# Kernel optimization log

Measured on AMD Instinct MI355X. Metric: run time of the kernel, lower is better.

The kernel has to match this reference:

```python
import jax, jax.numpy as jnp
import numpy as np

B, S, D, H = 2, 2048, 2048, 16
HD = D // H  # 128 head dim


def setup_inputs() -> dict:
    key = jax.random.key(0)
    k1, k2, k3 = jax.random.split(key, 3)
    x = jax.random.normal(k1, (B, S, D), dtype=jnp.float32)
    w_qkv = jax.random.normal(k2, (3 * D, D), dtype=jnp.float32) * 0.02
    w_out = jax.random.normal(k3, (D, D), dtype=jnp.float32) * 0.02
    # complex-like RoPE table: freqs_cis[s, j] = exp(i * s * theta^{-2j/hd})
    theta = 10000.0
    inv_freq = 1.0 / (theta ** (jnp.arange(0, HD, 2, dtype=jnp.float32) / HD))  # [HD/2]
    t = jnp.arange(S, dtype=jnp.float32)
    freqs = jnp.outer(t, inv_freq)  # [S, HD/2]
    return {"x": x, "w_qkv": w_qkv, "w_out": w_out,
            "freqs_cos": jnp.cos(freqs), "freqs_sin": jnp.sin(freqs)}


def _apply_rope(t, cos, sin):
    # t: [b, s, h, hd]; adjacent pairs treated as complex (real, imag)
    b, s, h, hd = t.shape
    tr = t.reshape(b, s, h, hd // 2, 2)
    re, im = tr[..., 0], tr[..., 1]
    c = cos[None, :, None, :]  # [1, s, 1, hd/2]
    sn = sin[None, :, None, :]
    out_re = re * c - im * sn
    out_im = re * sn + im * c
    return jnp.stack([out_re, out_im], axis=-1).reshape(b, s, h, hd)


def reference(x, w_qkv, w_out, freqs_cos, freqs_sin):
    b, s, d = x.shape
    qkv = x @ w_qkv.T  # [b, s, 3d]
    q, k, v = jnp.split(qkv, 3, axis=-1)
    q = q.reshape(b, s, H, HD)
    k = k.reshape(b, s, H, HD)
    v = v.reshape(b, s, H, HD)
    q = _apply_rope(q, freqs_cos, freqs_sin)
    k = _apply_rope(k, freqs_cos, freqs_sin)
    # causal SDPA
    scale = 1.0 / jnp.sqrt(jnp.asarray(HD, dtype=x.dtype))
    scores = jnp.einsum("bqhd,bkhd->bhqk", q, k) * scale  # [b, h, s, s]
    causal = jnp.tril(jnp.ones((s, s), dtype=bool))
    scores = jnp.where(causal[None, None], scores, jnp.finfo(scores.dtype).min)
    attn = jax.nn.softmax(scores, axis=-1)
    out = jnp.einsum("bhqk,bkhd->bqhd", attn, v).reshape(b, s, d)
    return out @ w_out.T
```

## Files before the change

kernel.cpp:

```cpp
#include <hip/hip_runtime.h>
#include <hip/hip_bf16.h>
#include <stdint.h>

#define S_ 2048
#define D_ 2048
#define H_ 16
#define HD_ 128

typedef __bf16 bf16x8 __attribute__((ext_vector_type(8)));
typedef float f32x4 __attribute__((ext_vector_type(4)));
typedef unsigned short ushort_t;
typedef ushort_t us4 __attribute__((ext_vector_type(4)));

__device__ __forceinline__ float bf2f(ushort_t u) {
  union { float f; uint32_t i; } x; x.i = ((uint32_t)u) << 16; return x.f;
}
__device__ __forceinline__ ushort_t f2bf(float f) {
  union { float f; uint32_t i; } x; x.f = f;
  uint32_t r = x.i + 0x7fffu + ((x.i >> 16) & 1u);
  return (ushort_t)(r >> 16);
}

__device__ __forceinline__ void async_copy16(const void* g, void* l) {
  __builtin_amdgcn_global_load_lds(
      (const __attribute__((address_space(1))) unsigned int*)g,
      (__attribute__((address_space(3))) unsigned int*)l, 16, 0, 0);
}

__device__ __forceinline__ void store_val(float* p, float v) { *p = v; }
__device__ __forceinline__ void store_val(ushort_t* p, float v) { *p = f2bf(v); }

__global__ __launch_bounds__(256) void cvt_f32_bf16(const float* __restrict__ in,
                                                    ushort_t* __restrict__ out,
                                                    int n4) {
  int i = blockIdx.x * 256 + threadIdx.x;
  if (i >= n4) return;
  const float4 v = ((const float4*)in)[i];
  us4 o;
  o.x = f2bf(v.x); o.y = f2bf(v.y); o.z = f2bf(v.z); o.w = f2bf(v.w);
  ((us4*)out)[i] = o;
}

template <typename OutT>
__global__ __launch_bounds__(256) void gemm_bt(const ushort_t* __restrict__ A,
                                               const ushort_t* __restrict__ Bm,
                                               OutT* __restrict__ C,
                                               int M, int N, int K) {
  __shared__ __align__(16) ushort_t As[128 * 32];
  __shared__ __align__(16) ushort_t Bs[128 * 32];
  const int tid = threadIdx.x;
  const int wave = tid >> 6, lane = tid & 63;
  const int quad = lane >> 4, l16 = lane & 15;
  const int bm = blockIdx.y * 128, bn = blockIdx.x * 128;
  const int wm = (wave >> 1) * 64, wn = (wave & 1) * 64;

  f32x4 acc[4][4] = {};

  const int c0 = wave * 2, c1 = c0 + 1;
  const int srow = lane >> 2;
  const int scol = (lane & 3) * 8;
  const ushort_t* gA0 = A + (size_t)(bm + c0 * 16 + srow) * K + scol;
  const ushort_t* gA1 = A + (size_t)(bm + c1 * 16 + srow) * K + scol;
  const ushort_t* gB0 = Bm + (size_t)(bn + c0 * 16 + srow) * K + scol;
  const ushort_t* gB1 = Bm + (size_t)(bn + c1 * 16 + srow) * K + scol;
  ushort_t* lA0 = As + c0 * 512;
  ushort_t* lA1 = As + c1 * 512;
  ushort_t* lB0 = Bs + c0 * 512;
  ushort_t* lB1 = Bs + c1 * 512;

  for (int k0 = 0; k0 < K; k0 += 32) {
    __syncthreads();
    async_copy16(gA0 + k0, lA0);
    async_copy16(gA1 + k0, lA1);
    async_copy16(gB0 + k0, lB0);
    async_copy16(gB1 + k0, lB1);
    __syncthreads();
    bf16x8 af[4], bfr[4];
#pragma unroll
    for (int i = 0; i < 4; ++i)
      af[i] = *(const bf16x8*)(As + (wm + i * 16 + l16) * 32 + quad * 8);
#pragma unroll
    for (int i = 0; i < 4; ++i)
      bfr[i] = *(const bf16x8*)(Bs + (wn + i * 16 + l16) * 32 + quad * 8);
#pragma unroll
    for (int mi = 0; mi < 4; ++mi)
#pragma unroll
      for (int ni = 0; ni < 4; ++ni)
        acc[mi][ni] = __builtin_amdgcn_mfma_f32_16x16x32_bf16(af[mi], bfr[ni],
                                                              acc[mi][ni], 0, 0, 0);
  }
#pragma unroll
  for (int mi = 0; mi < 4; ++mi)
#pragma unroll
    for (int ni = 0; ni < 4; ++ni)
#pragma unroll
      for (int r = 0; r < 4; ++r) {
        int row = bm + wm + mi * 16 + quad * 4 + r;
        int col = bn + wn + ni * 16 + l16;
        store_val(&C[(size_t)row * N + col], acc[mi][ni][r]);
      }
}

__global__ __launch_bounds__(256) void rope_k(ushort_t* __restrict__ qkv,
                                              const float* __restrict__ fc,
                                              const float* __restrict__ fs) {
  int idx = blockIdx.x * 256 + threadIdx.x;
  int i = idx & 63;
  int hh = (idx >> 6) & 15;
  int m = idx >> 10;
  int s = m & (S_ - 1);
  float c = fc[s * 64 + i], sn = fs[s * 64 + i];
  size_t off = (size_t)m * (3 * D_) + hh * HD_ + 2 * i;
#pragma unroll
  for (int part = 0; part < 2; ++part) {
    uint32_t* p = (uint32_t*)(qkv + off + part * D_);
    uint32_t v = *p;
    float re = bf2f((ushort_t)(v & 0xffffu));
    float im = bf2f((ushort_t)(v >> 16));
    float nr = re * c - im * sn;
    float ni = re * sn + im * c;
    *p = (uint32_t)f2bf(nr) | ((uint32_t)f2bf(ni) << 16);
  }
}

__global__ __launch_bounds__(256) void vt_prep(const ushort_t* __restrict__ qkv,
                                               ushort_t* __restrict__ VTg) {
  __shared__ __align__(16) ushort_t T[64 * 136];
  const int st = blockIdx.x, h = blockIdx.y, b = blockIdx.z;
  const int tid = threadIdx.x;
  const ushort_t* gV = qkv + (size_t)(b * S_ + st * 64) * (3 * D_) + 2 * D_ + h * HD_;
  {
    const int r = tid >> 2, cc = (tid & 3) * 32;
    const ushort_t* src = gV + (size_t)r * (3 * D_) + cc;
    uint4 a0 = ((const uint4*)src)[0];
    uint4 a1 = ((const uint4*)src)[1];
    uint4 a2 = ((const uint4*)src)[2];
    uint4 a3 = ((const uint4*)src)[3];
    ushort_t* dst = T + r * 136 + cc;
    ((uint4*)dst)[0] = a0; ((uint4*)dst)[1] = a1;
    ((uint4*)dst)[2] = a2; ((uint4*)dst)[3] = a3;
  }
  __syncthreads();
  const int d = tid >> 1, kh = (tid & 1) * 32;
  ushort_t buf[32];
#pragma unroll
  for (int j = 0; j < 32; ++j) buf[j] = T[(kh + j) * 136 + d];
  ushort_t* out = VTg + ((size_t)((b * H_ + h) * HD_ + d)) * S_ + st * 64 + kh;
  ((uint4*)out)[0] = *(const uint4*)(buf + 0);
  ((uint4*)out)[1] = *(const uint4*)(buf + 8);
  ((uint4*)out)[2] = *(const uint4*)(buf + 16);
  ((uint4*)out)[3] = *(const uint4*)(buf + 24);
}

#define SOFTMAX_C 12.0f

__global__ __launch_bounds__(256, 4) void attn_fwd(const ushort_t* __restrict__ qkv,
                                                   const ushort_t* __restrict__ VTg,
                                                   float* __restrict__ Oacc,
                                                   float* __restrict__ lsum_g) {
  __shared__ __align__(16) ushort_t Kl[64 * 128];
  __shared__ __align__(16) ushort_t VT[128 * 64];
  __shared__ __align__(16) ushort_t Pl[4 * 16 * 64];

  const int j = 79 - (int)blockIdx.x;
  int qt, c;
  if (j < 8)       { qt = j;                 c = 0; }
  else if (j < 24) { int t = j - 8;  qt = 8 + (t >> 1);  c = t & 1; }
  else if (j < 48) { int t = j - 24; qt = 16 + t / 3;    c = t % 3; }
  else             { int t = j - 48; qt = 24 + (t >> 2); c = t & 3; }
  const int h = blockIdx.y, b = blockIdx.z;
  const int kt0 = c * 8;
  const int kt_end = min(kt0 + 8, qt + 1);

  const int tid = threadIdx.x;
  const int wave = tid >> 6, lane = tid & 63;
  const int quad = lane >> 4, l16 = lane & 15;
  const float scale = 0.08838834764831845f;

  const int qg = qt * 64 + wave * 16 + l16;
  const ushort_t* qrow = qkv + (size_t)(b * S_ + qg) * (3 * D_) + h * HD_;
  bf16x8 qf[4];
#pragma unroll
  for (int cc = 0; cc < 4; ++cc)
    qf[cc] = *(const bf16x8*)(qrow + cc * 32 + quad * 8);

  f32x4 o[8] = {};
  float lsum[4] = {0.f, 0.f, 0.f, 0.f};
  const int q_row_base = qt * 64 + wave * 16 + quad * 4;
  ushort_t* Pw = Pl + wave * 16 * 64;

  const ushort_t* gK = qkv + (size_t)(b * S_) * (3 * D_) + D_ + h * HD_;
  const ushort_t* gVT = VTg + (size_t)(b * H_ + h) * HD_ * S_;

  const int krow_off = lane >> 4;
  const int kchunk = lane & 15;
  const int vrow_off = lane >> 3;
  const int vchunk = lane & 7;

  for (int kt = kt0; kt < kt_end; ++kt) {
    __syncthreads();
#pragma unroll
    for (int i = 0; i < 4; ++i) {
      int row = wave * 16 + i * 4 + krow_off;
      int lchunk = kchunk ^ (row & 15);
      async_copy16(gK + (size_t)(kt * 64 + row) * (3 * D_) + lchunk * 8,
                   Kl + (wave * 16 + i * 4) * 128);
    }
#pragma unroll
    for (int i = 0; i < 4; ++i) {
      int row = wave * 32 + i * 8 + vrow_off;
      int lchunk = vchunk ^ (row & 7);
      async_copy16(gVT + (size_t)row * S_ + kt * 64 + lchunk * 8,
                   VT + (wave * 32 + i * 8) * 64);
    }
    __syncthreads();

    const bool diag = (kt == qt);
#pragma unroll
    for (int g = 0; g < 4; ++g) {
      f32x4 s = {0.f, 0.f, 0.f, 0.f};
#pragma unroll
      for (int cc = 0; cc < 4; ++cc) {
        bf16x8 kf = *(const bf16x8*)(Kl + (g * 16 + l16) * 128 +
                                     (((cc * 4 + quad) ^ l16) * 8));
        s = __builtin_amdgcn_mfma_f32_16x16x32_bf16(qf[cc], kf, s, 0, 0, 0);
      }
      const int key = kt * 64 + g * 16 + l16;
#pragma unroll
      for (int r = 0; r < 4; ++r) {
        float e = __expf(s[r] * scale - SOFTMAX_C);
        float p = (!diag || key <= q_row_base + r) ? e : 0.f;
        lsum[r] += p;
        int prow = quad * 4 + r;
        int pcol = g * 16 + l16;
        Pw[prow * 64 + (((pcol >> 3) ^ (prow & 7)) * 8) + (pcol & 7)] = f2bf(p);
      }
    }
    bf16x8 pf0 = *(const bf16x8*)(Pw + l16 * 64 + ((quad ^ (l16 & 7)) * 8));
    bf16x8 pf1 = *(const bf16x8*)(Pw + l16 * 64 + (((4 + quad) ^ (l16 & 7)) * 8));
#pragma unroll
    for (int dc = 0; dc < 8; ++dc) {
      bf16x8 v0 = *(const bf16x8*)(VT + (dc * 16 + l16) * 64 +
                                   (((0 * 4 + quad) ^ (l16 & 7)) * 8));
      o[dc] = __builtin_amdgcn_mfma_f32_16x16x32_bf16(pf0, v0, o[dc], 0, 0, 0);
      bf16x8 v1 = *(const bf16x8*)(VT + (dc * 16 + l16) * 64 +
                                   (((1 * 4 + quad) ^ (l16 & 7)) * 8));
      o[dc] = __builtin_amdgcn_mfma_f32_16x16x32_bf16(pf1, v1, o[dc], 0, 0, 0);
    }
  }

#pragma unroll
  for (int r = 0; r < 4; ++r) {
    float l = lsum[r];
    l += __shfl_xor(l, 1, 64);
    l += __shfl_xor(l, 2, 64);
    l += __shfl_xor(l, 4, 64);
    l += __shfl_xor(l, 8, 64);
    size_t row = (size_t)(b * S_ + q_row_base + r);
    if (l16 == 0) unsafeAtomicAdd(&lsum_g[row * H_ + h], l);
#pragma unroll
    for (int dc = 0; dc < 8; ++dc)
      unsafeAtomicAdd(&Oacc[row * D_ + h * HD_ + dc * 16 + l16], o[dc][r]);
  }
}

__global__ __launch_bounds__(256) void combine(const float* __restrict__ Oacc,
                                               const float* __restrict__ lsum_g,
                                               ushort_t* __restrict__ attn) {
  int i = blockIdx.x * 256 + threadIdx.x;
  float4 v = ((const float4*)Oacc)[i];
  int flat = i * 4;
  int row = flat >> 11;
  int h = (flat >> 7) & 15;
  float inv = 1.0f / lsum_g[row * H_ + h];
  us4 o;
  o.x = f2bf(v.x * inv); o.y = f2bf(v.y * inv);
  o.z = f2bf(v.z * inv); o.w = f2bf(v.w * inv);
  ((us4*)attn)[i] = o;
}

extern "C" void kernel_launch(void* const* d_in, const int* in_sizes, int n_in,
                              void* d_out, int out_size, void* d_ws, size_t ws_size,
                              hipStream_t stream) {
  const float* x = (const float*)d_in[0];
  const float* w_qkv = (const float*)d_in[1];
  const float* w_out = (const float*)d_in[2];
  const float* fcos = (const float*)d_in[3];
  const float* fsin = (const float*)d_in[4];
  float* out = (float*)d_out;

  char* ws = (char*)d_ws;
  ushort_t* x_bf    = (ushort_t*)(ws + 0);
  ushort_t* wqkv_bf = (ushort_t*)(ws + 16777216);
  ushort_t* wout_bf = (ushort_t*)(ws + 41943040);
  ushort_t* qkv     = (ushort_t*)(ws + 50331648);
  ushort_t* attn    = (ushort_t*)(ws + 100663296);
  float* Oacc   = (float*)(ws + 0);
  float* lsum_g = (float*)(ws + 33554432);
  ushort_t* VTg = (ushort_t*)(ws + 100663296);

  cvt_f32_bf16<<<8192, 256, 0, stream>>>(x, x_bf, 2097152);
  cvt_f32_bf16<<<12288, 256, 0, stream>>>(w_qkv, wqkv_bf, 3145728);
  cvt_f32_bf16<<<4096, 256, 0, stream>>>(w_out, wout_bf, 1048576);

  gemm_bt<ushort_t><<<dim3(48, 32), 256, 0, stream>>>(x_bf, wqkv_bf, qkv,
                                                      4096, 6144, 2048);
  rope_k<<<16384, 256, 0, stream>>>(qkv, fcos, fsin);
  vt_prep<<<dim3(32, 16, 2), 256, 0, stream>>>(qkv, VTg);

  hipMemsetAsync(Oacc, 0, 33554432, stream);
  hipMemsetAsync(lsum_g, 0, 262144, stream);

  attn_fwd<<<dim3(80, 16, 2), 256, 0, stream>>>(qkv, VTg, Oacc, lsum_g);
  combine<<<8192, 256, 0, stream>>>(Oacc, lsum_g, attn);

  gemm_bt<float><<<dim3(16, 32), 256, 0, stream>>>(attn, wout_bf, out,
                                                   4096, 2048, 2048);
}
```

Before: 466.1 us.

## Add 256x256 double-buffered async-LDS GEMM for the QKV projection

Adds a new bf16 GEMM kernel with 256x256 block tiles, 512 threads and K-steps of 64. It stages tiles through double-buffered LDS with asynchronous global-to-LDS copies and an XOR swizzle against bank conflicts. The main loop is split into four MFMA phases, with prefetch of the next tile interleaved between them and wave priority raised around the MFMAs. Only the QKV projection uses it. The goal is more data reuse per tile and overlap of loads with compute, at the cost of 128KB of LDS per block, which limits occupancy, and a grid of 384 blocks that leaves an uneven tail.

Measured after the change: 453.9 us. 1.03x faster.

```diff
diff --git a/kernel.cpp b/kernel.cpp
--- a/kernel.cpp
+++ b/kernel.cpp
@@ -91,6 +91,159 @@
   }
 #pragma unroll
   for (int mi = 0; mi < 4; ++mi)
+#pragma unroll
+    for (int ni = 0; ni < 4; ++ni)
+#pragma unroll
+      for (int r = 0; r < 4; ++r) {
+        int row = bm + wm + mi * 16 + quad * 4 + r;
+        int col = bn + wn + ni * 16 + l16;
+        store_val(&C[(size_t)row * N + col], acc[mi][ni][r]);
+      }
+}
+
+__device__ __forceinline__ void stage_half(const ushort_t* __restrict__ g, int K,
+                                           ushort_t* l, int wave, int srow,
+                                           int clog) {
+#pragma unroll
+  for (int i = 0; i < 2; ++i)
+    async_copy16(g + (size_t)(i * 64 + srow) * K + clog * 8,
+                 l + wave * 512 + i * 4096);
+}
+
+#define MFMA_BF16(a, b, c) __builtin_amdgcn_mfma_f32_16x16x32_bf16(a, b, c, 0, 0, 0)
+
+template <typename OutT>
+__global__ __launch_bounds__(512, 2) void gemm_bt256(const ushort_t* __restrict__ A,
+                                                     const ushort_t* __restrict__ Bm,
+                                                     OutT* __restrict__ C,
+                                                     int M, int N, int K) {
+  __shared__ __align__(16) ushort_t As[2][256 * 64];
+  __shared__ __align__(16) ushort_t Bs[2][256 * 64];
+  const int tid = threadIdx.x;
+  const int wave = tid >> 6, lane = tid & 63;
+  const int quad = lane >> 4, l16 = lane & 15;
+  const int bm = blockIdx.y * 256, bn = blockIdx.x * 256;
+  const int wm = (wave >> 2) * 128;
+  const int wn = (wave & 3) * 64;
+  const int srow = tid >> 3;
+  const int clog = (tid & 7) ^ (srow & 7);
+  const int ck0 = (quad ^ (l16 & 7)) * 8;
+  const int ck1 = ((4 + quad) ^ (l16 & 7)) * 8;
+
+  const ushort_t* gA = A + (size_t)bm * K;
+  const ushort_t* gB = Bm + (size_t)bn * K;
+  const int NT = K >> 6;
+
+  f32x4 acc[8][4] = {};
+
+  stage_half(gA, K, &As[0][0], wave, srow, clog);
+  stage_half(gA + (size_t)128 * K, K, &As[0][8192], wave, srow, clog);
+  stage_half(gB, K, &Bs[0][0], wave, srow, clog);
+  stage_half(gB + (size_t)128 * K, K, &Bs[0][8192], wave, srow, clog);
+  if (NT > 1) {
+    stage_half(gA + 64, K, &As[1][0], wave, srow, clog);
+    asm volatile("s_waitcnt vmcnt(2)" ::: "memory");
+  } else {
+    asm volatile("s_waitcnt vmcnt(0)" ::: "memory");
+  }
+  __builtin_amdgcn_sched_barrier(0);
+  __builtin_amdgcn_s_barrier();
+
+  for (int t = 0; t < NT; ++t) {
+    const ushort_t* A_cur = &As[t & 1][0];
+    const ushort_t* B_cur = &Bs[t & 1][0];
+    ushort_t* A_nxt = &As[(t + 1) & 1][0];
+    ushort_t* B_nxt = &Bs[(t + 1) & 1][0];
+    const ushort_t* Arow = A_cur + (wm + l16) * 64;
+    const ushort_t* Brow = B_cur + (wn + l16) * 64;
+    const size_t kn = (size_t)(t + 1) * 64;
+    const bool pf1 = (t + 1 < NT);
+    const bool pf2 = (t + 2 < NT);
+
+    bf16x8 a4[4][2], b01[2][2], b23[2][2];
+
+#pragma unroll
+    for (int mi = 0; mi < 4; ++mi) {
+      a4[mi][0] = *(const bf16x8*)(Arow + mi * 1024 + ck0);
+      a4[mi][1] = *(const bf16x8*)(Arow + mi * 1024 + ck1);
+    }
+#pragma unroll
+    for (int ni = 0; ni < 2; ++ni) {
+      b01[ni][0] = *(const bf16x8*)(Brow + ni * 1024 + ck0);
+      b01[ni][1] = *(const bf16x8*)(Brow + ni * 1024 + ck1);
+    }
+    if (pf1) stage_half(gA + (size_t)128 * K + kn, K, A_nxt + 8192, wave, srow, clog);
+    __builtin_amdgcn_s_barrier();
+    __builtin_amdgcn_s_setprio(1);
+#pragma unroll
+    for (int mi = 0; mi < 4; ++mi)
+#pragma unroll
+      for (int ni = 0; ni < 2; ++ni) {
+        acc[mi][ni] = MFMA_BF16(a4[mi][0], b01[ni][0], acc[mi][ni]);
+        acc[mi][ni] = MFMA_BF16(a4[mi][1], b01[ni][1], acc[mi][ni]);
+      }
+    __builtin_amdgcn_s_setprio(0);
+    __builtin_amdgcn_s_barrier();
+
+#pragma unroll
+    for (int ni = 0; ni < 2; ++ni) {
+      b23[ni][0] = *(const bf16x8*)(Brow + (ni + 2) * 1024 + ck0);
+      b23[ni][1] = *(const bf16x8*)(Brow + (ni + 2) * 1024 + ck1);
+    }
+    if (pf1) stage_half(gB + kn, K, B_nxt, wave, srow, clog);
+    __builtin_amdgcn_s_barrier();
+    __builtin_amdgcn_s_setprio(1);
+#pragma unroll
+    for (int mi = 0; mi < 4; ++mi)
+#pragma unroll
+      for (int ni = 0; ni < 2; ++ni) {
+        acc[mi][ni + 2] = MFMA_BF16(a4[mi][0], b23[ni][0], acc[mi][ni + 2]);
+        acc[mi][ni + 2] = MFMA_BF16(a4[mi][1], b23[ni][1], acc[mi][ni + 2]);
+      }
+    __builtin_amdgcn_s_setprio(0);
+    __builtin_amdgcn_s_barrier();
+
+#pragma unroll
+    for (int mi = 0; mi < 4; ++mi) {
+      a4[mi][0] = *(const bf16x8*)(Arow + (mi + 4) * 1024 + ck0);
+      a4[mi][1] = *(const bf16x8*)(Arow + (mi + 4) * 1024 + ck1);
+    }
+    if (pf1) stage_half(gB + (size_t)128 * K + kn, K, B_nxt + 8192, wave, srow, clog);
+    __builtin_amdgcn_s_barrier();
+    __builtin_amdgcn_s_setprio(1);
+#pragma unroll
+    for (int mi = 0; mi < 4; ++mi)
+#pragma unroll
+      for (int ni = 0; ni < 2; ++ni) {
+        acc[mi + 4][ni] = MFMA_BF16(a4[mi][0], b01[ni][0], acc[mi + 4][ni]);
+        acc[mi + 4][ni] = MFMA_BF16(a4[mi][1], b01[ni][1], acc[mi + 4][ni]);
+      }
+    __builtin_amdgcn_s_setprio(0);
+    __builtin_amdgcn_s_barrier();
+
+    if (pf2) {
+      stage_half(gA + (size_t)(t + 2) * 64, K, (ushort_t*)A_cur, wave, srow, clog);
+      asm volatile("s_waitcnt vmcnt(2)" ::: "memory");
+    } else {
+      asm volatile("s_waitcnt vmcnt(0)" ::: "memory");
+    }
+    __builtin_amdgcn_sched_barrier(0);
+    __builtin_amdgcn_s_barrier();
+    __builtin_amdgcn_s_setprio(1);
+#pragma unroll
+    for (int mi = 0; mi < 4; ++mi)
+#pragma unroll
+      for (int ni = 0; ni < 2; ++ni) {
+        acc[mi + 4][ni + 2] = MFMA_BF16(a4[mi][0], b23[ni][0], acc[mi + 4][ni + 2]);
+        acc[mi + 4][ni + 2] = MFMA_BF16(a4[mi][1], b23[ni][1], acc[mi + 4][ni + 2]);
+      }
+    __builtin_amdgcn_s_setprio(0);
+    __builtin_amdgcn_s_barrier();
+    __builtin_amdgcn_sched_barrier(0);
+  }
+
+#pragma unroll
+  for (int mi = 0; mi < 8; ++mi)
 #pragma unroll
     for (int ni = 0; ni < 4; ++ni)
 #pragma unroll
@@ -303,8 +456,8 @@
   cvt_f32_bf16<<<12288, 256, 0, stream>>>(w_qkv, wqkv_bf, 3145728);
   cvt_f32_bf16<<<4096, 256, 0, stream>>>(w_out, wout_bf, 1048576);
 
-  gemm_bt<ushort_t><<<dim3(48, 32), 256, 0, stream>>>(x_bf, wqkv_bf, qkv,
-                                                      4096, 6144, 2048);
+  gemm_bt256<ushort_t><<<dim3(24, 16), 512, 0, stream>>>(x_bf, wqkv_bf, qkv,
+                                                         4096, 6144, 2048);
   rope_k<<<16384, 256, 0, stream>>>(qkv, fcos, fsin);
   vt_prep<<<dim3(32, 16, 2), 256, 0, stream>>>(qkv, VTg);
 
```
